# Optimization experiments

Measured on AMD Instinct MI355X. Metric: run time of the kernel, lower is better.

Reference implementation:

```python
import jax, jax.numpy as jnp
import numpy as np

EMB = 768
HEADS = 12
HEAD_DIM = EMB // HEADS


def setup_inputs() -> dict:
    key = jax.random.key(0)
    k1, k2, k3, k4 = jax.random.split(key, 4)
    x = jax.random.normal(k1, (8, 1024, EMB), dtype=jnp.float32)
    # Dense kernels, TF default glorot-ish scale approximated with small normals
    w_qkv = jax.random.normal(k2, (EMB, 3 * EMB), dtype=jnp.float32) * 0.02
    w_out = jax.random.normal(k3, (EMB, EMB), dtype=jnp.float32) * 0.02
    b_out = jnp.zeros((EMB,), dtype=jnp.float32)
    return {"x": x, "w_qkv": w_qkv, "w_out": w_out, "b_out": b_out}


def reference(x, w_qkv, w_out, b_out):
    B, S, E = x.shape
    qkv = jnp.einsum("bse,ef->bsf", x, w_qkv)                 # [B,S,3E]
    qkv = qkv.reshape(B, S, 3, HEADS, HEAD_DIM)
    qkv = jnp.transpose(qkv, (2, 0, 3, 1, 4))                  # [3,B,H,S,D]
    q, k, v = qkv[0], qkv[1], qkv[2]
    scale = jnp.float32(HEAD_DIM) ** -0.5
    # Blocked loop in source computes exact full (non-causal) attention:
    # every query block attends to all keys -> equivalent to standard SDPA.
    scores = jnp.einsum("bhqd,bhkd->bhqk", q, k) * scale       # [B,H,S,S]
    probs = jax.nn.softmax(scores, axis=-1)
    out = jnp.einsum("bhqk,bhkd->bhqd", probs, v)              # [B,H,S,D]
    out = jnp.transpose(out, (0, 2, 1, 3)).reshape(B, S, E)
    return jnp.einsum("bse,ef->bsf", out, w_out) + b_out
```

## Files before the change

kernel.cpp:

```cpp
#include <hip/hip_runtime.h>

typedef float f32x4 __attribute__((ext_vector_type(4)));
typedef short bf16x8 __attribute__((ext_vector_type(8)));

#define MFMA_BF16(a, b, c) __builtin_amdgcn_mfma_f32_16x16x32_bf16((a), (b), (c), 0, 0, 0)

#define GLDS16(gp, lp) __builtin_amdgcn_global_load_lds( \
    (const __attribute__((address_space(1))) unsigned int*)(gp), \
    (__attribute__((address_space(3))) unsigned int*)(lp), 16, 0, 0)

__device__ __forceinline__ ushort f2bf(float f) {
    unsigned int u = __float_as_uint(f);
    return (ushort)((u + 0x7FFFu + ((u >> 16) & 1u)) >> 16);
}

__device__ __forceinline__ float fexp2(float x) {
#if __has_builtin(__builtin_amdgcn_exp2f)
    return __builtin_amdgcn_exp2f(x);
#else
    return exp2f(x);
#endif
}

__global__ __launch_bounds__(256) void prep_kernel(
    const float* __restrict__ x, const float* __restrict__ wq, const float* __restrict__ wo,
    ushort* __restrict__ xb, ushort* __restrict__ wqbt, ushort* __restrict__ wobt)
{
    __shared__ float tile[32][33];
    const int bid = blockIdx.x;
    if (bid < 2048) {
        const float4* src = (const float4*)x;
        ushort4* dst = (ushort4*)xb;
        for (int i = bid * 256 + threadIdx.x; i < 1572864; i += 2048 * 256) {
            float4 v = src[i];
            ushort4 o;
            o.x = f2bf(v.x); o.y = f2bf(v.y); o.z = f2bf(v.z); o.w = f2bf(v.w);
            dst[i] = o;
        }
        return;
    }
    const float* src; ushort* dst; int K, N, bx, by;
    if (bid < 3776) {
        const int L = bid - 2048;
        src = wq; dst = wqbt; K = 768; N = 2304; bx = L % 72; by = L / 72;
    } else {
        const int L = bid - 3776;
        src = wo; dst = wobt; K = 768; N = 768; bx = L % 24; by = L / 24;
    }
    const int n0 = bx * 32, k0 = by * 32;
    const int c = threadIdx.x & 31, rb = threadIdx.x >> 5;
    #pragma unroll
    for (int i = 0; i < 4; ++i)
        tile[i * 8 + rb][c] = src[(size_t)(k0 + i * 8 + rb) * N + n0 + c];
    __syncthreads();
    #pragma unroll
    for (int i = 0; i < 4; ++i) {
        int nr = i * 8 + rb;
        dst[(size_t)(n0 + nr) * K + k0 + c] = f2bf(tile[c][nr]);
    }
}

__global__ __launch_bounds__(256) void gemm_qkv_mfma(
    const ushort* __restrict__ A, const ushort* __restrict__ Bt,
    ushort* __restrict__ Qo, ushort* __restrict__ Ko, ushort* __restrict__ Vo)
{
    __shared__ ushort Al[2][8192];
    __shared__ ushort Bl[2][8192];
    const int tid = threadIdx.x, lane = tid & 63;
    const int wv = tid >> 6, lo = lane & 15, hi = lane >> 4;
    const int wr = wv >> 1, wc = wv & 1;
    const int L = blockIdx.x;
    const int nid = (L & 7) * 144 + (L >> 3);
    const int n0 = (nid % 18) * 128, m0 = (nid / 18) * 128;

    auto stage = [&](int bi, int k0) {
        #pragma unroll
        for (int it = 0; it < 4; ++it) {
            const int p = it * 256 + tid;
            const int row = p >> 3, ch = (p & 7) ^ (row & 7);
            GLDS16(A + (size_t)(m0 + row) * 768 + k0 + ch * 8,
                   &Al[bi][(it * 256 + (tid & 192)) * 8]);
        }
        #pragma unroll
        for (int it = 0; it < 4; ++it) {
            const int p = it * 256 + tid;
            const int row = p >> 3, ch = (p & 7) ^ (row & 7);
            GLDS16(Bt + (size_t)(n0 + row) * 768 + k0 + ch * 8,
                   &Bl[bi][(it * 256 + (tid & 192)) * 8]);
        }
    };

    f32x4 acc[4][4];
    #pragma unroll
    for (int i = 0; i < 4; ++i)
        #pragma unroll
        for (int j = 0; j < 4; ++j)
            acc[i][j] = (f32x4){0.f, 0.f, 0.f, 0.f};

    const int region = n0 / 768;
    const int h = ((n0 % 768) >> 6) + wc;

    stage(0, 0);
    stage(1, 64);

    int cur = 0;
    for (int t = 0; t < 12; ++t) {
        if (t < 11) asm volatile("s_waitcnt vmcnt(8)" ::: "memory");
        else        asm volatile("s_waitcnt vmcnt(0)" ::: "memory");
        __builtin_amdgcn_s_barrier();
        asm volatile("" ::: "memory");

        #pragma unroll
        for (int ks = 0; ks < 2; ++ks) {
            bf16x8 af[4], bfr[4];
            #pragma unroll
            for (int i = 0; i < 4; ++i) {
                const int ra = wr * 64 + i * 16 + lo;
                af[i] = *(const bf16x8*)&Al[cur][ra * 64 + (((ks * 4 + hi) ^ (ra & 7)) * 8)];
                const int rb = wc * 64 + i * 16 + lo;
                bfr[i] = *(const bf16x8*)&Bl[cur][rb * 64 + (((ks * 4 + hi) ^ (rb & 7)) * 8)];
            }
            if (region == 2) {
                #pragma unroll
                for (int mi = 0; mi < 4; ++mi)
                    #pragma unroll
                    for (int nj = 0; nj < 4; ++nj)
                        acc[mi][nj] = MFMA_BF16(af[mi], bfr[nj], acc[mi][nj]);
            } else {
                #pragma unroll
                for (int mi = 0; mi < 4; ++mi)
                    #pragma unroll
                    for (int nj = 0; nj < 4; ++nj)
                        acc[mi][nj] = MFMA_BF16(bfr[nj], af[mi], acc[mi][nj]);
            }
        }

        asm volatile("s_waitcnt lgkmcnt(0)" ::: "memory");
        __builtin_amdgcn_s_barrier();
        asm volatile("" ::: "memory");
        if (t + 2 < 12) stage(cur, (t + 2) * 64);
        cur ^= 1;
    }

    if (region == 2) {
        #pragma unroll
        for (int mi = 0; mi < 4; ++mi) {
            const int m4 = m0 + wr * 64 + mi * 16 + hi * 4;
            const int b = m4 >> 10, s = m4 & 1023;
            #pragma unroll
            for (int nj = 0; nj < 4; ++nj) {
                const int d = nj * 16 + lo;
                ushort4 pk;
                pk.x = f2bf(acc[mi][nj][0]); pk.y = f2bf(acc[mi][nj][1]);
                pk.z = f2bf(acc[mi][nj][2]); pk.w = f2bf(acc[mi][nj][3]);
                *(ushort4*)&Vo[((size_t)(b * 12 + h) * 64 + d) * 1024 + s] = pk;
            }
        }
    } else {
        ushort* dst = region ? Ko : Qo;
        const float sc = region ? 1.0f : 0.18033688011112042f;
        #pragma unroll
        for (int mi = 0; mi < 4; ++mi) {
            const int s_idx = m0 + wr * 64 + mi * 16 + lo;
            const int b = s_idx >> 10, s = s_idx & 1023;
            const size_t base = ((size_t)(b * 12 + h) * 1024 + s) * 64;
            #pragma unroll
            for (int nj = 0; nj < 4; ++nj) {
                ushort4 pk;
                pk.x = f2bf(acc[mi][nj][0] * sc); pk.y = f2bf(acc[mi][nj][1] * sc);
                pk.z = f2bf(acc[mi][nj][2] * sc); pk.w = f2bf(acc[mi][nj][3] * sc);
                *(ushort4*)&dst[base + nj * 16 + hi * 4] = pk;
            }
        }
    }
}

__global__ __launch_bounds__(256) void attn_mfma_kernel(
    const ushort* __restrict__ Qg, const ushort* __restrict__ Kg,
    const ushort* __restrict__ Vg, ushort* __restrict__ AO)
{
    __shared__ ushort Kl[2][4096];
    __shared__ ushort Vl[2][4096];
    __shared__ ushort Pl[4][32 * 72];

    const int tid = threadIdx.x, lane = tid & 63;
    const int wv = tid >> 6, lo = lane & 15, hi = lane >> 4;
    const int L = blockIdx.x;
    const int xcd = L & 7, g = L >> 3;
    const int qb = g / 12;
    const int bh = xcd * 12 + (g % 12);
    const int b = bh / 12, h = bh % 12;
    const size_t kvbase = (size_t)bh * (1024 * 64);

    bf16x8 qa[2][2];
    const int qrow0 = qb * 128 + wv * 32;
    #pragma unroll
    for (int mi = 0; mi < 2; ++mi)
        #pragma unroll
        for (int ks = 0; ks < 2; ++ks)
            qa[mi][ks] = *(const bf16x8*)&Qg[kvbase + (size_t)(qrow0 + mi * 16 + lo) * 64 + ks * 32 + hi * 8];

    f32x4 o[2][4];
    float lp[2] = {0.f, 0.f};
    #pragma unroll
    for (int mi = 0; mi < 2; ++mi)
        #pragma unroll
        for (int dj = 0; dj < 4; ++dj) o[mi][dj] = (f32x4){0.f, 0.f, 0.f, 0.f};

    auto stage = [&](int bi, int kt) {
        #pragma unroll
        for (int it = 0; it < 2; ++it) {
            const int p = it * 256 + tid;
            const int row = p >> 3, ch = (p & 7) ^ (row & 7);
            GLDS16(Kg + kvbase + (size_t)(kt + row) * 64 + ch * 8, &Kl[bi][(it * 256 + (tid & 192)) * 8]);
        }
        #pragma unroll
        for (int it = 0; it < 2; ++it) {
            const int p = it * 256 + tid;
            const int row = p >> 3, ch = (p & 7) ^ (row & 7);
            GLDS16(Vg + kvbase + (size_t)row * 1024 + kt + ch * 8, &Vl[bi][(it * 256 + (tid & 192)) * 8]);
        }
    };

    stage(0, 0);
    __syncthreads();

    for (int t = 0; t < 16; ++t) {
        const int cur = t & 1;
        if (t < 15) stage(cur ^ 1, (t + 1) * 64);

        f32x4 s[2][4];
        #pragma unroll
        for (int mi = 0; mi < 2; ++mi)
            #pragma unroll
            for (int nj = 0; nj < 4; ++nj) s[mi][nj] = (f32x4){0.f, 0.f, 0.f, 0.f};
        #pragma unroll
        for (int ks = 0; ks < 2; ++ks) {
            bf16x8 kb[4];
            #pragma unroll
            for (int nj = 0; nj < 4; ++nj) {
                const int key = nj * 16 + lo, c = ks * 4 + hi;
                kb[nj] = *(const bf16x8*)&Kl[cur][key * 64 + ((c ^ (key & 7)) * 8)];
            }
            #pragma unroll
            for (int mi = 0; mi < 2; ++mi)
                #pragma unroll
                for (int nj = 0; nj < 4; ++nj)
                    s[mi][nj] = MFMA_BF16(kb[nj], qa[mi][ks], s[mi][nj]);
        }

        #pragma unroll
        for (int mi = 0; mi < 2; ++mi) {
            #pragma unroll
            for (int nj = 0; nj < 4; ++nj) {
                const unsigned int u0 = __float_as_uint(fexp2(s[mi][nj][0]));
                const unsigned int u1 = __float_as_uint(fexp2(s[mi][nj][1]));
                const unsigned int u2 = __float_as_uint(fexp2(s[mi][nj][2]));
                const unsigned int u3 = __float_as_uint(fexp2(s[mi][nj][3]));
                const float t0 = __uint_as_float(u0 & 0xFFFF0000u);
                const float t1 = __uint_as_float(u1 & 0xFFFF0000u);
                const float t2 = __uint_as_float(u2 & 0xFFFF0000u);
                const float t3 = __uint_as_float(u3 & 0xFFFF0000u);
                lp[mi] += (t0 + t1) + (t2 + t3);
                ushort4 pk;
                pk.x = (ushort)(u0 >> 16); pk.y = (ushort)(u1 >> 16);
                pk.z = (ushort)(u2 >> 16); pk.w = (ushort)(u3 >> 16);
                *(ushort4*)&Pl[wv][(mi * 16 + lo) * 72 + nj * 16 + hi * 4] = pk;
            }
        }

        #pragma unroll
        for (int ks = 0; ks < 2; ++ks) {
            bf16x8 pa[2];
            #pragma unroll
            for (int mi = 0; mi < 2; ++mi)
                pa[mi] = *(const bf16x8*)&Pl[wv][(mi * 16 + lo) * 72 + ks * 32 + hi * 8];
            bf16x8 vb[4];
            #pragma unroll
            for (int dj = 0; dj < 4; ++dj) {
                const int d = dj * 16 + lo, c = ks * 4 + hi;
                vb[dj] = *(const bf16x8*)&Vl[cur][d * 64 + ((c ^ (d & 7)) * 8)];
            }
            #pragma unroll
            for (int mi = 0; mi < 2; ++mi)
                #pragma unroll
                for (int dj = 0; dj < 4; ++dj)
                    o[mi][dj] = MFMA_BF16(pa[mi], vb[dj], o[mi][dj]);
        }
        __syncthreads();
    }

    #pragma unroll
    for (int mi = 0; mi < 2; ++mi) {
        float l = lp[mi];
        l += __shfl_xor(l, 16);
        l += __shfl_xor(l, 32);
        #pragma unroll
        for (int r = 0; r < 4; ++r) {
            const float lr = __shfl(l, hi * 4 + r, 16);
            const float rcp = 1.0f / lr;
            const int srow = qrow0 + mi * 16 + hi * 4 + r;
            #pragma unroll
            for (int dj = 0; dj < 4; ++dj)
                AO[((size_t)(b * 1024 + srow)) * 768 + h * 64 + dj * 16 + lo] =
                    f2bf(o[mi][dj][r] * rcp);
        }
    }
}

__global__ __launch_bounds__(256) void gemm_out_mfma(
    const ushort* __restrict__ A, const ushort* __restrict__ Bt,
    const float* __restrict__ bias, float* __restrict__ C)
{
    __shared__ ushort Al[2][8192];
    __shared__ ushort Bl[2][8192];
    const int tid = threadIdx.x, lane = tid & 63;
    const int wv = tid >> 6, lo = lane & 15, hi = lane >> 4;
    const int wr = wv >> 1, wc = wv & 1;
    const int L = blockIdx.x;
    const int nid = (L & 7) * 48 + (L >> 3);
    const int n0 = (nid % 6) * 128, m0 = (nid / 6) * 128;

    auto stage = [&](int bi, int k0) {
        #pragma unroll
        for (int it = 0; it < 4; ++it) {
            const int p = it * 256 + tid;
            const int row = p >> 3, ch = (p & 7) ^ (row & 7);
            GLDS16(A + (size_t)(m0 + row) * 768 + k0 + ch * 8,
                   &Al[bi][(it * 256 + (tid & 192)) * 8]);
        }
        #pragma unroll
        for (int it = 0; it < 4; ++it) {
            const int p = it * 256 + tid;
            const int row = p >> 3, ch = (p & 7) ^ (row & 7);
            GLDS16(Bt + (size_t)(n0 + row) * 768 + k0 + ch * 8,
                   &Bl[bi][(it * 256 + (tid & 192)) * 8]);
        }
    };

    f32x4 acc[4][4];
    #pragma unroll
    for (int i = 0; i < 4; ++i)
        #pragma unroll
        for (int j = 0; j < 4; ++j)
            acc[i][j] = (f32x4){0.f, 0.f, 0.f, 0.f};

    stage(0, 0);
    stage(1, 64);

    int cur = 0;
    for (int t = 0; t < 12; ++t) {
        if (t < 11) asm volatile("s_waitcnt vmcnt(8)" ::: "memory");
        else        asm volatile("s_waitcnt vmcnt(0)" ::: "memory");
        __builtin_amdgcn_s_barrier();
        asm volatile("" ::: "memory");

        #pragma unroll
        for (int ks = 0; ks < 2; ++ks) {
            bf16x8 af[4], bfr[4];
            #pragma unroll
            for (int i = 0; i < 4; ++i) {
                const int ra = wr * 64 + i * 16 + lo;
                af[i] = *(const bf16x8*)&Al[cur][ra * 64 + (((ks * 4 + hi) ^ (ra & 7)) * 8)];
                const int rb = wc * 64 + i * 16 + lo;
                bfr[i] = *(const bf16x8*)&Bl[cur][rb * 64 + (((ks * 4 + hi) ^ (rb & 7)) * 8)];
            }
            #pragma unroll
            for (int mi = 0; mi < 4; ++mi)
                #pragma unroll
                for (int nj = 0; nj < 4; ++nj)
                    acc[mi][nj] = MFMA_BF16(bfr[nj], af[mi], acc[mi][nj]);
        }

        asm volatile("s_waitcnt lgkmcnt(0)" ::: "memory");
        __builtin_amdgcn_s_barrier();
        asm volatile("" ::: "memory");
        if (t + 2 < 12) stage(cur, (t + 2) * 64);
        cur ^= 1;
    }

    const int ncol0 = n0 + wc * 64;
    #pragma unroll
    for (int mi = 0; mi < 4; ++mi) {
        const int m = m0 + wr * 64 + mi * 16 + lo;
        #pragma unroll
        for (int nj = 0; nj < 4; ++nj) {
            const int nb = ncol0 + nj * 16 + hi * 4;
            const float4 bv = *reinterpret_cast<const float4*>(&bias[nb]);
            float4 ov;
            ov.x = acc[mi][nj][0] + bv.x; ov.y = acc[mi][nj][1] + bv.y;
            ov.z = acc[mi][nj][2] + bv.z; ov.w = acc[mi][nj][3] + bv.w;
            *reinterpret_cast<float4*>(&C[(size_t)m * 768 + nb]) = ov;
        }
    }
}

extern "C" void kernel_launch(void* const* d_in, const int* in_sizes, int n_in,
                              void* d_out, int out_size, void* d_ws, size_t ws_size,
                              hipStream_t stream) {
    const float* x     = (const float*)d_in[0];
    const float* w_qkv = (const float*)d_in[1];
    const float* w_out = (const float*)d_in[2];
    const float* b_out = (const float*)d_in[3];
    float* out = (float*)d_out;

    (void)in_sizes; (void)n_in; (void)out_size; (void)ws_size;

    ushort* xb   = (ushort*)d_ws;
    ushort* wqbt = xb + 6291456;
    ushort* wobt = wqbt + 1769472;
    ushort* Qs   = wobt + 589824;
    ushort* Ks   = Qs + 6291456;
    ushort* Vt   = Ks + 6291456;
    ushort* AO   = Vt + 6291456;

    prep_kernel<<<4352, 256, 0, stream>>>(x, w_qkv, w_out, xb, wqbt, wobt);
    gemm_qkv_mfma<<<1152, 256, 0, stream>>>(xb, wqbt, Qs, Ks, Vt);
    attn_mfma_kernel<<<768, 256, 0, stream>>>(Qs, Ks, Vt, AO);
    gemm_out_mfma<<<384, 256, 0, stream>>>(AO, wobt, b_out, out);
}
```

Before: 122.9 us.

## Use triple-buffered BK=32 pipeline in GEMMs, raise MFMA priority in attention

Both projection GEMMs switch from double-buffered BK=64 stages to three LDS buffers of BK=32. This removes the second barrier per iteration: the prefetch for stage s+2 is issued right after the single barrier, into the buffer consumed two steps earlier. The LDS swizzle changes to a 4-chunk XOR pattern to match the narrower rows. The attention kernel wraps its MFMA blocks in s_setprio(1)/s_setprio(0) so matrix issue gets priority over other waves. There are now twice as many loop iterations and barriers per GEMM, and each stage carries less work to hide latency.

```diff
diff --git a/kernel.cpp b/kernel.cpp
--- a/kernel.cpp
+++ b/kernel.cpp
@@ -64,8 +64,8 @@
     const ushort* __restrict__ A, const ushort* __restrict__ Bt,
     ushort* __restrict__ Qo, ushort* __restrict__ Ko, ushort* __restrict__ Vo)
 {
-    __shared__ ushort Al[2][8192];
-    __shared__ ushort Bl[2][8192];
+    __shared__ ushort Al[3][4096];
+    __shared__ ushort Bl[3][4096];
     const int tid = threadIdx.x, lane = tid & 63;
     const int wv = tid >> 6, lo = lane & 15, hi = lane >> 4;
     const int wr = wv >> 1, wc = wv & 1;
@@ -73,19 +73,20 @@
     const int nid = (L & 7) * 144 + (L >> 3);
     const int n0 = (nid % 18) * 128, m0 = (nid / 18) * 128;
 
-    auto stage = [&](int bi, int k0) {
-        #pragma unroll
-        for (int it = 0; it < 4; ++it) {
-            const int p = it * 256 + tid;
-            const int row = p >> 3, ch = (p & 7) ^ (row & 7);
-            GLDS16(A + (size_t)(m0 + row) * 768 + k0 + ch * 8,
+    auto stage = [&](int bi, int s) {
+        const int k0 = s * 32;
+        #pragma unroll
+        for (int it = 0; it < 2; ++it) {
+            const int p = it * 256 + tid;
+            const int row = p >> 2, c = p & 3;
+            GLDS16(A + (size_t)(m0 + row) * 768 + k0 + ((c ^ (row & 3)) * 8),
                    &Al[bi][(it * 256 + (tid & 192)) * 8]);
         }
         #pragma unroll
-        for (int it = 0; it < 4; ++it) {
-            const int p = it * 256 + tid;
-            const int row = p >> 3, ch = (p & 7) ^ (row & 7);
-            GLDS16(Bt + (size_t)(n0 + row) * 768 + k0 + ch * 8,
+        for (int it = 0; it < 2; ++it) {
+            const int p = it * 256 + tid;
+            const int row = p >> 2, c = p & 3;
+            GLDS16(Bt + (size_t)(n0 + row) * 768 + k0 + ((c ^ (row & 3)) * 8),
                    &Bl[bi][(it * 256 + (tid & 192)) * 8]);
         }
     };
@@ -101,59 +102,52 @@
     const int h = ((n0 % 768) >> 6) + wc;
 
     stage(0, 0);
-    stage(1, 64);
+    stage(1, 1);
 
     int cur = 0;
-    for (int t = 0; t < 12; ++t) {
-        if (t < 11) asm volatile("s_waitcnt vmcnt(8)" ::: "memory");
+    for (int s = 0; s < 24; ++s) {
+        if (s < 23) asm volatile("s_waitcnt vmcnt(4)" ::: "memory");
         else        asm volatile("s_waitcnt vmcnt(0)" ::: "memory");
         __builtin_amdgcn_s_barrier();
         asm volatile("" ::: "memory");
-
-        #pragma unroll
-        for (int ks = 0; ks < 2; ++ks) {
-            bf16x8 af[4], bfr[4];
-            #pragma unroll
-            for (int i = 0; i < 4; ++i) {
-                const int ra = wr * 64 + i * 16 + lo;
-                af[i] = *(const bf16x8*)&Al[cur][ra * 64 + (((ks * 4 + hi) ^ (ra & 7)) * 8)];
-                const int rb = wc * 64 + i * 16 + lo;
-                bfr[i] = *(const bf16x8*)&Bl[cur][rb * 64 + (((ks * 4 + hi) ^ (rb & 7)) * 8)];
-            }
-            if (region == 2) {
+        if (s + 2 < 24) stage(cur == 0 ? 2 : cur - 1, s + 2);
+
+        bf16x8 af[4], bfr[4];
+        #pragma unroll
+        for (int i = 0; i < 4; ++i) {
+            const int ra = wr * 64 + i * 16 + lo;
+            af[i] = *(const bf16x8*)&Al[cur][ra * 32 + ((hi ^ (ra & 3)) * 8)];
+            const int rb = wc * 64 + i * 16 + lo;
+            bfr[i] = *(const bf16x8*)&Bl[cur][rb * 32 + ((hi ^ (rb & 3)) * 8)];
+        }
+        if (region == 2) {
+            #pragma unroll
+            for (int mi = 0; mi < 4; ++mi)
                 #pragma unroll
-                for (int mi = 0; mi < 4; ++mi)
-                    #pragma unroll
-                    for (int nj = 0; nj < 4; ++nj)
-                        acc[mi][nj] = MFMA_BF16(af[mi], bfr[nj], acc[mi][nj]);
-            } else {
+                for (int nj = 0; nj < 4; ++nj)
+                    acc[mi][nj] = MFMA_BF16(af[mi], bfr[nj], acc[mi][nj]);
+        } else {
+            #pragma unroll
+            for (int mi = 0; mi < 4; ++mi)
                 #pragma unroll
-                for (int mi = 0; mi < 4; ++mi)
-                    #pragma unroll
-                    for (int nj = 0; nj < 4; ++nj)
-                        acc[mi][nj] = MFMA_BF16(bfr[nj], af[mi], acc[mi][nj]);
-            }
-        }
-
-        asm volatile("s_waitcnt lgkmcnt(0)" ::: "memory");
-        __builtin_amdgcn_s_barrier();
-        asm volatile("" ::: "memory");
-        if (t + 2 < 12) stage(cur, (t + 2) * 64);
-        cur ^= 1;
+                for (int nj = 0; nj < 4; ++nj)
+                    acc[mi][nj] = MFMA_BF16(bfr[nj], af[mi], acc[mi][nj]);
+        }
+        cur = (cur == 2) ? 0 : cur + 1;
     }
 
     if (region == 2) {
         #pragma unroll
         for (int mi = 0; mi < 4; ++mi) {
             const int m4 = m0 + wr * 64 + mi * 16 + hi * 4;
-            const int b = m4 >> 10, s = m4 & 1023;
+            const int b = m4 >> 10, sx = m4 & 1023;
             #pragma unroll
             for (int nj = 0; nj < 4; ++nj) {
                 const int d = nj * 16 + lo;
                 ushort4 pk;
                 pk.x = f2bf(acc[mi][nj][0]); pk.y = f2bf(acc[mi][nj][1]);
                 pk.z = f2bf(acc[mi][nj][2]); pk.w = f2bf(acc[mi][nj][3]);
-                *(ushort4*)&Vo[((size_t)(b * 12 + h) * 64 + d) * 1024 + s] = pk;
+                *(ushort4*)&Vo[((size_t)(b * 12 + h) * 64 + d) * 1024 + sx] = pk;
             }
         }
     } else {
@@ -162,8 +156,8 @@
         #pragma unroll
         for (int mi = 0; mi < 4; ++mi) {
             const int s_idx = m0 + wr * 64 + mi * 16 + lo;
-            const int b = s_idx >> 10, s = s_idx & 1023;
-            const size_t base = ((size_t)(b * 12 + h) * 1024 + s) * 64;
+            const int b = s_idx >> 10, sx = s_idx & 1023;
+            const size_t base = ((size_t)(b * 12 + h) * 1024 + sx) * 64;
             #pragma unroll
             for (int nj = 0; nj < 4; ++nj) {
                 ushort4 pk;
@@ -242,11 +236,13 @@
                 const int key = nj * 16 + lo, c = ks * 4 + hi;
                 kb[nj] = *(const bf16x8*)&Kl[cur][key * 64 + ((c ^ (key & 7)) * 8)];
             }
+            __builtin_amdgcn_s_setprio(1);
             #pragma unroll
             for (int mi = 0; mi < 2; ++mi)
                 #pragma unroll
                 for (int nj = 0; nj < 4; ++nj)
                     s[mi][nj] = MFMA_BF16(kb[nj], qa[mi][ks], s[mi][nj]);
+            __builtin_amdgcn_s_setprio(0);
         }
 
         #pragma unroll
@@ -281,11 +277,13 @@
                 const int d = dj * 16 + lo, c = ks * 4 + hi;
                 vb[dj] = *(const bf16x8*)&Vl[cur][d * 64 + ((c ^ (d & 7)) * 8)];
             }
+            __builtin_amdgcn_s_setprio(1);
             #pragma unroll
             for (int mi = 0; mi < 2; ++mi)
                 #pragma unroll
                 for (int dj = 0; dj < 4; ++dj)
                     o[mi][dj] = MFMA_BF16(pa[mi], vb[dj], o[mi][dj]);
+            __builtin_amdgcn_s_setprio(0);
         }
         __syncthreads();
     }
@@ -312,8 +310,8 @@
     const ushort* __restrict__ A, const ushort* __restrict__ Bt,
     const float* __restrict__ bias, float* __restrict__ C)
 {
-    __shared__ ushort Al[2][8192];
-    __shared__ ushort Bl[2][8192];
+    __shared__ ushort Al[3][4096];
+    __shared__ ushort Bl[3][4096];
     const int tid = threadIdx.x, lane = tid & 63;
     const int wv = tid >> 6, lo = lane & 15, hi = lane >> 4;
     const int wr = wv >> 1, wc = wv & 1;
@@ -321,19 +319,20 @@
     const int nid = (L & 7) * 48 + (L >> 3);
     const int n0 = (nid % 6) * 128, m0 = (nid / 6) * 128;
 
-    auto stage = [&](int bi, int k0) {
-        #pragma unroll
-        for (int it = 0; it < 4; ++it) {
-            const int p = it * 256 + tid;
-            const int row = p >> 3, ch = (p & 7) ^ (row & 7);
-            GLDS16(A + (size_t)(m0 + row) * 768 + k0 + ch * 8,
+    auto stage = [&](int bi, int s) {
+        const int k0 = s * 32;
+        #pragma unroll
+        for (int it = 0; it < 2; ++it) {
+            const int p = it * 256 + tid;
+            const int row = p >> 2, c = p & 3;
+            GLDS16(A + (size_t)(m0 + row) * 768 + k0 + ((c ^ (row & 3)) * 8),
                    &Al[bi][(it * 256 + (tid & 192)) * 8]);
         }
         #pragma unroll
-        for (int it = 0; it < 4; ++it) {
-            const int p = it * 256 + tid;
-            const int row = p >> 3, ch = (p & 7) ^ (row & 7);
-            GLDS16(Bt + (size_t)(n0 + row) * 768 + k0 + ch * 8,
+        for (int it = 0; it < 2; ++it) {
+            const int p = it * 256 + tid;
+            const int row = p >> 2, c = p & 3;
+            GLDS16(Bt + (size_t)(n0 + row) * 768 + k0 + ((c ^ (row & 3)) * 8),
                    &Bl[bi][(it * 256 + (tid & 192)) * 8]);
         }
     };
@@ -346,37 +345,30 @@
             acc[i][j] = (f32x4){0.f, 0.f, 0.f, 0.f};
 
     stage(0, 0);
-    stage(1, 64);
+    stage(1, 1);
 
     int cur = 0;
-    for (int t = 0; t < 12; ++t) {
-        if (t < 11) asm volatile("s_waitcnt vmcnt(8)" ::: "memory");
+    for (int s = 0; s < 24; ++s) {
+        if (s < 23) asm volatile("s_waitcnt vmcnt(4)" ::: "memory");
         else        asm volatile("s_waitcnt vmcnt(0)" ::: "memory");
         __builtin_amdgcn_s_barrier();
         asm volatile("" ::: "memory");
-
-        #pragma unroll
-        for (int ks = 0; ks < 2; ++ks) {
-            bf16x8 af[4], bfr[4];
-            #pragma unroll
-            for (int i = 0; i < 4; ++i) {
-                const int ra = wr * 64 + i * 16 + lo;
-                af[i] = *(const bf16x8*)&Al[cur][ra * 64 + (((ks * 4 + hi) ^ (ra & 7)) * 8)];
-                const int rb = wc * 64 + i * 16 + lo;
-                bfr[i] = *(const bf16x8*)&Bl[cur][rb * 64 + (((ks * 4 + hi) ^ (rb & 7)) * 8)];
-            }
-            #pragma unroll
-            for (int mi = 0; mi < 4; ++mi)
-                #pragma unroll
-                for (int nj = 0; nj < 4; ++nj)
-                    acc[mi][nj] = MFMA_BF16(bfr[nj], af[mi], acc[mi][nj]);
-        }
-
-        asm volatile("s_waitcnt lgkmcnt(0)" ::: "memory");
-        __builtin_amdgcn_s_barrier();
-        asm volatile("" ::: "memory");
-        if (t + 2 < 12) stage(cur, (t + 2) * 64);
-        cur ^= 1;
+        if (s + 2 < 24) stage(cur == 0 ? 2 : cur - 1, s + 2);
+
+        bf16x8 af[4], bfr[4];
+        #pragma unroll
+        for (int i = 0; i < 4; ++i) {
+            const int ra = wr * 64 + i * 16 + lo;
+            af[i] = *(const bf16x8*)&Al[cur][ra * 32 + ((hi ^ (ra & 3)) * 8)];
+            const int rb = wc * 64 + i * 16 + lo;
+            bfr[i] = *(const bf16x8*)&Bl[cur][rb * 32 + ((hi ^ (rb & 3)) * 8)];
+        }
+        #pragma unroll
+        for (int mi = 0; mi < 4; ++mi)
+            #pragma unroll
+            for (int nj = 0; nj < 4; ++nj)
+                acc[mi][nj] = MFMA_BF16(bfr[nj], af[mi], acc[mi][nj]);
+        cur = (cur == 2) ? 0 : cur + 1;
     }
 
     const int ncol0 = n0 + wc * 64;
```

Result: slower. 145.1 us (+18.1%).
